# Kernel tuning notes

Hardware: AMD Instinct MI355X
Metric: run time of the kernel (lower is better)

The kernel has to match this reference:

```python
import jax, jax.numpy as jnp
import numpy as np

B, L, D = 4, 2048, 1024
NUM_HEADS = 1
HEAD_DIM = D // NUM_HEADS  # 1024


def setup_inputs() -> dict:
    key = jax.random.key(0)
    ks = jax.random.split(key, 12)
    s = 1.0 / np.sqrt(D)
    return {
        "query": jax.random.normal(ks[0], (B, L, D), jnp.float32),
        "key": jax.random.normal(ks[1], (B, L, D), jnp.float32),
        "value": jax.random.normal(ks[2], (B, L, D), jnp.float32),
        "mask": jax.random.randint(ks[3], (B, 1, L, L), 0, 2, jnp.int32),
        "Wq": jax.random.uniform(ks[4], (D, D * NUM_HEADS), jnp.float32, -s, s),
        "bq": jnp.zeros((D * NUM_HEADS,), jnp.float32),
        "Wk": jax.random.uniform(ks[5], (D, D * NUM_HEADS), jnp.float32, -s, s),
        "bk": jnp.zeros((D * NUM_HEADS,), jnp.float32),
        "Wv": jax.random.uniform(ks[6], (D, D * NUM_HEADS), jnp.float32, -s, s),
        "bv": jnp.zeros((D * NUM_HEADS,), jnp.float32),
        "Wo": jax.random.uniform(ks[7], (D * NUM_HEADS, D), jnp.float32, -s, s),
        "bo": jnp.zeros((D,), jnp.float32),
    }


def reference(query, key, value, mask, Wq, bq, Wk, bk, Wv, bv, Wo, bo):
    b, lq = query.shape[0], query.shape[1]
    lk = key.shape[1]
    # project and split heads: (B, L, H, Dh) -> (B, H, L, Dh)
    Q = (query @ Wq + bq).reshape(b, lq, NUM_HEADS, HEAD_DIM).transpose(0, 2, 1, 3)
    K = (key @ Wk + bk).reshape(b, lk, NUM_HEADS, HEAD_DIM).transpose(0, 2, 1, 3)
    V = (value @ Wv + bv).reshape(b, lk, NUM_HEADS, HEAD_DIM).transpose(0, 2, 1, 3)
    scale = 1.0 / jnp.sqrt(jnp.float32(HEAD_DIM))
    scores = jnp.einsum("bhqd,bhkd->bhqk", Q, K) * scale  # (B,H,Lq,Lk)
    scores = jnp.where(mask == 0, jnp.float32(-1e20), scores)
    attn = jax.nn.softmax(scores, axis=-1)
    out = jnp.einsum("bhqk,bhkd->bhqd", attn, V)  # (B,H,Lq,Dh)
    out = out.transpose(0, 2, 1, 3).reshape(b, lq, NUM_HEADS * HEAD_DIM)
    return out @ Wo + bo
```

## Files before the change

### kernel.cpp

```cpp
#include <hip/hip_runtime.h>

#define B_ 4
#define L_ 2048
#define D_ 1024
#define M_FLAT (B_*L_)
#define NE_ ((size_t)M_FLAT * D_)
#define WE_ ((size_t)D_ * D_)

typedef unsigned short bf16_t;
typedef __attribute__((ext_vector_type(8))) short bf16x8;
typedef __attribute__((ext_vector_type(4))) float f32x4;

__device__ __forceinline__ bf16_t f2bf(float f) {
  union { float f; unsigned int u; } c; c.f = f;
  unsigned int u = c.u;
  unsigned int r = (u + 0x7fffu + ((u >> 16) & 1u)) >> 16;
  return (bf16_t)r;
}
__device__ __forceinline__ float bf2f(bf16_t h) {
  union { unsigned int u; float f; } c; c.u = ((unsigned int)h) << 16;
  return c.f;
}

__device__ __forceinline__ void gload_lds16(const bf16_t* g, bf16_t* l) {
  __builtin_amdgcn_global_load_lds(
      (const __attribute__((address_space(1))) unsigned int*)g,
      (__attribute__((address_space(3))) unsigned int*)l, 16, 0, 0);
}

#define BARRIER() do { asm volatile("" ::: "memory"); \
                       __builtin_amdgcn_s_barrier();  \
                       asm volatile("" ::: "memory"); } while (0)

__global__ __launch_bounds__(256) void prep_cvt(const float* __restrict__ q,
                                                const float* __restrict__ k,
                                                const float* __restrict__ v,
                                                const float* __restrict__ wv,
                                                bf16_t* __restrict__ xq,
                                                bf16_t* __restrict__ wvb) {
  const float* in; bf16_t* out; size_t li;
  int b = blockIdx.x;
  if (b < 4096)       { in = q;  out = xq;            li = (size_t)b * 256 + threadIdx.x; }
  else if (b < 8192)  { in = k;  out = xq + NE_;      li = (size_t)(b - 4096) * 256 + threadIdx.x; }
  else if (b < 12288) { in = v;  out = xq + 2 * NE_;  li = (size_t)(b - 8192) * 256 + threadIdx.x; }
  else                { in = wv; out = wvb;           li = (size_t)(b - 12288) * 256 + threadIdx.x; }
  const float4* p = (const float4*)in + li * 2;
  float4 a = p[0], bb = p[1];
  union { bf16_t h[8]; uint4 u; } r;
  r.h[0] = f2bf(a.x); r.h[1] = f2bf(a.y); r.h[2] = f2bf(a.z); r.h[3] = f2bf(a.w);
  r.h[4] = f2bf(bb.x); r.h[5] = f2bf(bb.y); r.h[6] = f2bf(bb.z); r.h[7] = f2bf(bb.w);
  ((uint4*)out)[li] = r.u;
}

__global__ __launch_bounds__(256) void transpose_cvt3(const float* __restrict__ Wq,
                                                      const float* __restrict__ Wk,
                                                      const float* __restrict__ Wo,
                                                      bf16_t* __restrict__ outbase) {
  __shared__ float t[32][33];
  int zz = blockIdx.z;
  const float* Wsrc = (zz == 0) ? Wq : (zz == 1) ? Wk : Wo;
  bf16_t* Wt = outbase + (size_t)(zz == 2 ? 3 : zz) * WE_;
  int c0 = blockIdx.x * 32, r0 = blockIdx.y * 32;
  int tx = threadIdx.x, ty = threadIdx.y;
#pragma unroll
  for (int i = 0; i < 4; i++)
    t[ty + i * 8][tx] = Wsrc[(size_t)(r0 + ty + i * 8) * D_ + c0 + tx];
  __syncthreads();
#pragma unroll
  for (int i = 0; i < 4; i++)
    Wt[(size_t)(c0 + ty + i * 8) * D_ + r0 + tx] = f2bf(t[tx][ty + i * 8]);
}

__global__ __launch_bounds__(256) void c2_kernel(const float* __restrict__ bv,
                                                 const float* __restrict__ Wo,
                                                 float* __restrict__ c2) {
  int j = blockIdx.x * 256 + threadIdx.x;
  float s = 0.f;
  for (int k = 0; k < D_; k++) s += bv[k] * Wo[(size_t)k * D_ + j];
  c2[j] = s;
}

__global__ __launch_bounds__(256) void pack_mask(const int* __restrict__ mask,
                                                 unsigned long long* __restrict__ bm) {
  size_t gid = (size_t)blockIdx.x * 256 + threadIdx.x;
  int mi = mask[gid];
  unsigned long long b = __ballot(mi != 0);
  if ((threadIdx.x & 63) == 0) bm[gid >> 6] = b;
}

__global__ __launch_bounds__(256) void reduce_rsum(const float* __restrict__ rsp,
                                                   float* __restrict__ rs) {
  int r = blockIdx.x * 256 + threadIdx.x;
  float s = 0.f;
#pragma unroll
  for (int j = 0; j < 32; j++) s += rsp[(size_t)r * 32 + j];
  rs[r] = fmaxf(s, 1e-30f);
}

#define MODE_PROJ 0
#define MODE_S    1
#define MODE_FIN  2
#define MODE_TR   3

template <int BM, int MODE>
__global__ __launch_bounds__(512, 2)
void g8(const bf16_t* __restrict__ Abase, int lda, long strA,
        const bf16_t* __restrict__ Bbase, int ldb, long strB,
        void* __restrict__ outp, long strO, int ldo,
        const float* __restrict__ x0, const float* __restrict__ x1,
        const float* __restrict__ x2,
        const void* __restrict__ auxp, float* __restrict__ rsp,
        int K) {
  constexpr int WROWS = BM / 2;
  constexpr int QAF   = WROWS / 32;
  constexpr int MFR   = WROWS / 16;
  constexpr int AL    = BM / 128;
  constexpr int BL    = 2;
  constexpr int AHB   = WROWS * 128;
  constexpr int BUFB  = (BM + 256) * 128;
  extern __shared__ __align__(16) char smem[];

  const int tid = threadIdx.x, lane = tid & 63, w = tid >> 6;
  const int wm = w >> 2, wn = w & 3;
  const int fr = lane & 15, fs = lane >> 4;
  const int z = blockIdx.z;

  int gx = gridDim.x, nxy = gx * gridDim.y;
  int lin = blockIdx.y * gx + blockIdx.x;
  if ((nxy & 7) == 0) { int q = nxy >> 3; lin = (lin & 7) * q + (lin >> 3); }
  const int xb = lin % gx;
  const int mbase = (lin / gx) * BM, nbase = xb * 256;

  const bf16_t* A  = Abase + (size_t)z * strA;
  const bf16_t* Bt = Bbase + (size_t)z * strB;

  int offA[2][2], offB[2][2];
#pragma unroll
  for (int h = 0; h < 2; h++)
#pragma unroll
    for (int i = 0; i < 2; i++) {
      int c = i * 512 + tid, row = c >> 3;
      int sg = (c & 7) ^ (row & 7);
      if (i < AL) offA[h][i] = (mbase + h * WROWS + row) * lda + sg * 8;
      offB[h][i] = (nbase + h * 128 + row) * ldb + sg * 8;
    }

  const int swz0 = (fs ^ (fr & 7)) * 16;
  const int swz1 = ((4 + fs) ^ (fr & 7)) * 16;

  bf16x8 af[QAF][2], bfv[2][2][2];
  f32x4 acc[MFR][4] = {};

#define STAGE_A(h, kt, bsel) do {                                             \
    char* hb_ = smem + (bsel) * BUFB + (h) * AHB;                             \
    _Pragma("unroll")                                                         \
    for (int i_ = 0; i_ < AL; ++i_)                                           \
      gload_lds16(A + offA[h][i_] + (kt) * 64,                                \
                  (bf16_t*)(hb_ + (i_ * 512 + tid) * 16));                    \
  } while (0)
#define STAGE_B(h, kt, bsel) do {                                             \
    char* hb_ = smem + (bsel) * BUFB + BM * 128 + (h) * 16384;                \
    _Pragma("unroll")                                                         \
    for (int i_ = 0; i_ < BL; ++i_)                                           \
      gload_lds16(Bt + offB[h][i_] + (kt) * 64,                               \
                  (bf16_t*)(hb_ + (i_ * 512 + tid) * 16));                    \
  } while (0)
#define LOAD_A(bsel, mh) do {                                                 \
    const char* ab_ = smem + (bsel) * BUFB + (wm * WROWS) * 128;              \
    _Pragma("unroll")                                                         \
    for (int i_ = 0; i_ < QAF; ++i_) {                                        \
      int rb_ = ((mh) * (WROWS / 2) + i_ * 16 + fr) * 128;                    \
      af[i_][0] = *(const bf16x8*)(ab_ + rb_ + swz0);                         \
      af[i_][1] = *(const bf16x8*)(ab_ + rb_ + swz1);                         \
    }                                                                         \
  } while (0)
#define LOAD_B(bsel, nh) do {                                                 \
    const char* bb_ = smem + (bsel) * BUFB + BM * 128 + (wn * 64) * 128;      \
    _Pragma("unroll")                                                         \
    for (int j_ = 0; j_ < 2; ++j_) {                                          \
      int rb_ = ((nh) * 32 + j_ * 16 + fr) * 128;                             \
      bfv[nh][j_][0] = *(const bf16x8*)(bb_ + rb_ + swz0);                    \
      bfv[nh][j_][1] = *(const bf16x8*)(bb_ + rb_ + swz1);                    \
    }                                                                         \
  } while (0)
#define MFMA_Q(mh, nh) do {                                                   \
    __builtin_amdgcn_s_setprio(1);                                            \
    _Pragma("unroll")                                                         \
    for (int i_ = 0; i_ < QAF; ++i_)                                          \
    _Pragma("unroll")                                                         \
    for (int j_ = 0; j_ < 2; ++j_) {                                          \
      acc[(mh)*QAF + i_][(nh)*2 + j_] = __builtin_amdgcn_mfma_f32_16x16x32_bf16( \
          af[i_][0], bfv[nh][j_][0], acc[(mh)*QAF + i_][(nh)*2 + j_], 0, 0, 0);  \
      acc[(mh)*QAF + i_][(nh)*2 + j_] = __builtin_amdgcn_mfma_f32_16x16x32_bf16( \
          af[i_][1], bfv[nh][j_][1], acc[(mh)*QAF + i_][(nh)*2 + j_], 0, 0, 0);  \
    }                                                                         \
    __builtin_amdgcn_s_setprio(0);                                            \
  } while (0)
#define VMWN() do {                                                           \
    if constexpr (AL == 2) asm volatile("s_waitcnt vmcnt(8)" ::: "memory");   \
    else                   asm volatile("s_waitcnt vmcnt(6)" ::: "memory");   \
  } while (0)

  const int NK = K >> 6, NI = NK >> 1;

  STAGE_B(0, 0, 0); STAGE_B(1, 0, 0); STAGE_A(0, 0, 0); STAGE_A(1, 0, 0);
  STAGE_B(0, 1, 1); STAGE_B(1, 1, 1); STAGE_A(0, 1, 1); STAGE_A(1, 1, 1);
  VMWN(); BARRIER();

  for (int it = 0; it < NI; ++it) {
    const int ta = (2 * it + 2 < NK) ? 2 * it + 2 : NK - 1;
    const int tb = (2 * it + 3 < NK) ? 2 * it + 3 : NK - 1;
    LOAD_A(0, 0); LOAD_B(0, 0); MFMA_Q(0, 0);
    LOAD_B(0, 1);               MFMA_Q(0, 1);
    LOAD_A(0, 1);               MFMA_Q(1, 1);
                                MFMA_Q(1, 0);
    BARRIER();
    STAGE_B(0, ta, 0); STAGE_B(1, ta, 0); STAGE_A(0, ta, 0); STAGE_A(1, ta, 0);
    VMWN();
    BARRIER();
    LOAD_A(1, 0); LOAD_B(1, 0); MFMA_Q(0, 0);
    LOAD_B(1, 1);               MFMA_Q(0, 1);
    LOAD_A(1, 1);               MFMA_Q(1, 1);
                                MFMA_Q(1, 0);
    BARRIER();
    STAGE_B(0, tb, 1); STAGE_B(1, tb, 1); STAGE_A(0, tb, 1); STAGE_A(1, tb, 1);
    VMWN();
    BARRIER();
  }
  asm volatile("s_waitcnt vmcnt(0)" ::: "memory");

  const int r0 = mbase + wm * WROWS;
  const int c0 = nbase + wn * 64;

  if constexpr (MODE == MODE_PROJ) {
    BARRIER();
    char* ep = smem + w * AHB;
    if (z < 2) {
      bf16_t* o = (bf16_t*)outp + (size_t)z * strO;
      const float* bias = (z == 0) ? x0 : x1;
      const float scale = (z == 0) ? 0.03125f : 1.0f;
#pragma unroll
      for (int nf = 0; nf < 4; ++nf) {
        float bv = bias[c0 + nf * 16 + fr];
#pragma unroll
        for (int mf = 0; mf < MFR; ++mf)
#pragma unroll
          for (int jj = 0; jj < 4; ++jj) {
            int row = mf * 16 + fs * 4 + jj;
            int slot = (nf * 2 + (fr >> 3)) ^ ((row >> 1) & 7);
            *(bf16_t*)(ep + row * 128 + slot * 16 + (fr & 7) * 2) =
                f2bf((acc[mf][nf][jj] + bv) * scale);
          }
      }
      asm volatile("s_waitcnt lgkmcnt(0)" ::: "memory");
      const int rl = lane >> 3, sl = lane & 7;
#pragma unroll
      for (int i = 0; i < WROWS / 8; ++i) {
        int row = i * 8 + rl;
        int slot = sl ^ ((row >> 1) & 7);
        uint4 vv = *(const uint4*)(ep + row * 128 + slot * 16);
        *(uint4*)&o[(size_t)(r0 + row) * ldo + c0 + sl * 8] = vv;
      }
    } else {
      bf16_t* ob = (bf16_t*)auxp;
      const int bidx = r0 >> 11, rb = r0 & (L_ - 1);
      ob += (size_t)bidx * D_ * L_;
#pragma unroll
      for (int nf = 0; nf < 4; ++nf) {
        int coll = nf * 16 + fr;
        float bv = x2[c0 + coll];
        int xm = (coll & (WROWS / 8 - 1)) << 3;
#pragma unroll
        for (int mf = 0; mf < MFR; ++mf) {
          int rbase = mf * 16 + fs * 4;
          union { bf16_t h[4]; uint2 u; } pk;
#pragma unroll
          for (int jj = 0; jj < 4; ++jj) pk.h[jj] = f2bf(acc[mf][nf][jj] + bv);
          *(uint2*)(ep + coll * (WROWS * 2) + 2 * (rbase ^ xm)) = pk.u;
        }
      }
      asm volatile("s_waitcnt lgkmcnt(0)" ::: "memory");
      constexpr int LPC = WROWS / 8;
      constexpr int CPI = 64 / LPC;
      const int colr = lane / LPC;
      const int rc = (lane % LPC) * 8;
#pragma unroll
      for (int i2 = 0; i2 < LPC; ++i2) {
        int coll = i2 * CPI + colr;
        int xm = (coll & (WROWS / 8 - 1)) << 3;
        uint4 vv = *(const uint4*)(ep + coll * (WROWS * 2) + 2 * (rc ^ xm));
        *(uint4*)&ob[(size_t)(c0 + coll) * L_ + rb + rc] = vv;
      }
    }
  } else if constexpr (MODE == MODE_TR) {
    BARRIER();
    char* ep = smem + w * AHB;
    bf16_t* ob = (bf16_t*)outp;
#pragma unroll
    for (int nf = 0; nf < 4; ++nf) {
      int coll = nf * 16 + fr;
      int xm = (coll & (WROWS / 8 - 1)) << 3;
#pragma unroll
      for (int mf = 0; mf < MFR; ++mf) {
        int rbase = mf * 16 + fs * 4;
        union { bf16_t h[4]; uint2 u; } pk;
#pragma unroll
        for (int jj = 0; jj < 4; ++jj) pk.h[jj] = f2bf(acc[mf][nf][jj]);
        *(uint2*)(ep + coll * (WROWS * 2) + 2 * (rbase ^ xm)) = pk.u;
      }
    }
    asm volatile("s_waitcnt lgkmcnt(0)" ::: "memory");
    constexpr int LPC = WROWS / 8;
    constexpr int CPI = 64 / LPC;
    const int colr = lane / LPC;
    const int rc = (lane % LPC) * 8;
#pragma unroll
    for (int i2 = 0; i2 < LPC; ++i2) {
      int coll = i2 * CPI + colr;
      int xm = (coll & (WROWS / 8 - 1)) << 3;
      uint4 vv = *(const uint4*)(ep + coll * (WROWS * 2) + 2 * (rc ^ xm));
      *(uint4*)&ob[(size_t)(c0 + coll) * ldo + r0 + rc] = vv;
    }
  } else if constexpr (MODE == MODE_S) {
    BARRIER();
    char* ep = smem + w * AHB;
    bf16_t* o = (bf16_t*)outp + (size_t)z * strO;
    const unsigned long long* bw =
        (const unsigned long long*)auxp +
        ((size_t)z * L_ + r0) * 32 + (c0 >> 6);
#pragma unroll
    for (int mf = 0; mf < MFR; ++mf) {
#pragma unroll
      for (int jj = 0; jj < 4; ++jj) {
        int row = mf * 16 + fs * 4 + jj;
        unsigned long long wd = bw[(size_t)row * 32];
        float psum = 0.f;
#pragma unroll
        for (int nf = 0; nf < 4; ++nf) {
          int cbit = nf * 16 + fr;
          float e = ((wd >> cbit) & 1ull) ? __expf(acc[mf][nf][jj]) : 0.0f;
          bf16_t eb = f2bf(e);
          psum += bf2f(eb);
          int slot = (nf * 2 + (fr >> 3)) ^ ((row >> 1) & 7);
          *(bf16_t*)(ep + row * 128 + slot * 16 + (fr & 7) * 2) = eb;
        }
#pragma unroll
        for (int off = 8; off; off >>= 1) psum += __shfl_xor(psum, off, 16);
        if (fr == 0)
          rsp[((size_t)z * L_ + r0 + row) * 32 + xb * 4 + wn] = psum;
      }
    }
    asm volatile("s_waitcnt lgkmcnt(0)" ::: "memory");
    const int rl = lane >> 3, sl = lane & 7;
#pragma unroll
    for (int i = 0; i < WROWS / 8; ++i) {
      int row = i * 8 + rl;
      int slot = sl ^ ((row >> 1) & 7);
      uint4 vv = *(const uint4*)(ep + row * 128 + slot * 16);
      *(uint4*)&o[(size_t)(r0 + row) * ldo + c0 + sl * 8] = vv;
    }
  } else {
    float* o = (float*)outp + (size_t)z * strO;
    const float* rs = x0 + (size_t)z * L_;
#pragma unroll
    for (int mf = 0; mf < MFR; ++mf) {
#pragma unroll
      for (int jj = 0; jj < 4; ++jj) {
        int r = r0 + mf * 16 + fs * 4 + jj;
        float inv = 1.0f / rs[r];
#pragma unroll
        for (int nf = 0; nf < 4; ++nf) {
          int c = c0 + nf * 16 + fr;
          o[(size_t)r * ldo + c] = acc[mf][nf][jj] * inv + x1[c];
        }
      }
    }
  }
#undef STAGE_A
#undef STAGE_B
#undef LOAD_A
#undef LOAD_B
#undef MFMA_Q
#undef VMWN
}

extern "C" void kernel_launch(void* const* d_in, const int* in_sizes, int n_in,
                              void* d_out, int out_size, void* d_ws, size_t ws_size,
                              hipStream_t stream) {
  const float* query = (const float*)d_in[0];
  const float* keyi  = (const float*)d_in[1];
  const float* value = (const float*)d_in[2];
  const int*   mask  = (const int*)d_in[3];
  const float* Wq = (const float*)d_in[4];
  const float* bq = (const float*)d_in[5];
  const float* Wk = (const float*)d_in[6];
  const float* bk = (const float*)d_in[7];
  const float* Wv = (const float*)d_in[8];
  const float* bv = (const float*)d_in[9];
  const float* Wo = (const float*)d_in[10];
  const float* bo = (const float*)d_in[11];

  bf16_t* ws = (bf16_t*)d_ws;
  bf16_t* XQ   = ws;
  bf16_t* XK   = ws + NE_;
  bf16_t* XV   = ws + 2 * NE_;
  bf16_t* WQT  = ws + 3 * NE_;
  bf16_t* WKT  = WQT + WE_;
  bf16_t* W2T  = WKT + WE_;
  bf16_t* WOT  = W2T + WE_;
  bf16_t* WVb  = WOT + WE_;
  bf16_t* Qb   = WVb + WE_;
  bf16_t* Kb   = Qb + NE_;
  bf16_t* VWt  = Kb + NE_;
  float*  rsump= (float*)(VWt + NE_);
  float*  c2p  = rsump + (size_t)B_ * L_;
  float*  rspart = c2p + D_;
  unsigned long long* bmask =
      (unsigned long long*)(rspart + (size_t)B_ * L_ * 32);
  bf16_t* Sb   = ws;

  hipFuncSetAttribute((const void*)g8<128, MODE_PROJ>,
                      hipFuncAttributeMaxDynamicSharedMemorySize, 98304);
  hipFuncSetAttribute((const void*)g8<256, MODE_S>,
                      hipFuncAttributeMaxDynamicSharedMemorySize, 131072);
  hipFuncSetAttribute((const void*)g8<128, MODE_TR>,
                      hipFuncAttributeMaxDynamicSharedMemorySize, 98304);
  hipFuncSetAttribute((const void*)g8<128, MODE_FIN>,
                      hipFuncAttributeMaxDynamicSharedMemorySize, 98304);

  prep_cvt<<<dim3(12800), dim3(256), 0, stream>>>(query, keyi, value, Wv, XQ, WVb);
  pack_mask<<<dim3(65536), dim3(256), 0, stream>>>(mask, bmask);
  transpose_cvt3<<<dim3(32, 32, 3), dim3(32, 8), 0, stream>>>(Wq, Wk, Wo, WQT);
  c2_kernel<<<dim3(4), dim3(256), 0, stream>>>(bv, Wo, c2p);
  g8<128, MODE_TR><<<dim3(4, 8, 1), 512, 98304, stream>>>(
      WVb, D_, 0, WOT, D_, 0, W2T, 0, D_,
      nullptr, nullptr, nullptr, nullptr, nullptr, D_);
  g8<128, MODE_PROJ><<<dim3(4, 64, 3), 512, 98304, stream>>>(
      XQ, D_, (long)NE_, WQT, D_, (long)WE_, Qb, (long)NE_, D_,
      bq, bk, c2p, VWt, nullptr, D_);
  g8<256, MODE_S><<<dim3(8, 8, 4), 512, 131072, stream>>>(
      Qb, D_, (long)L_ * D_, Kb, D_, (long)L_ * D_, Sb, (long)L_ * L_, L_,
      nullptr, nullptr, nullptr, bmask, rspart, D_);
  reduce_rsum<<<dim3(32), dim3(256), 0, stream>>>(rspart, rsump);
  g8<128, MODE_FIN><<<dim3(4, 16, 4), 512, 98304, stream>>>(
      Sb, L_, (long)L_ * L_, VWt, L_, (long)D_ * L_, d_out, (long)L_ * D_, D_,
      rsump, bo, nullptr, nullptr, nullptr, L_);
}
```

Measured before the change: 264.2 us.

## Fuse fp32-to-bf16 input conversion into projection GEMM and split-K the Wv·Wo product

Removes the separate prep_cvt pass. The projection GEMM now loads the fp32 query/key/value tiles directly into registers, converts them to bf16 and writes them to LDS, so the extra read-write of bf16 copies of the inputs is gone. The small Wv·Wo weight-product GEMM, which previously ran on only 32 blocks, becomes an 8-way split-K into fp32 partials followed by a reduce-and-transpose kernel. Wv conversion moves into the weight transpose kernel. The trade-off is that A-tile staging now goes through registers and costs more VGPRs, with a heavier global-read path inside the main GEMM loop.

```diff
diff --git a/kernel.cpp b/kernel.cpp
--- a/kernel.cpp
+++ b/kernel.cpp
@@ -32,36 +32,26 @@
                        __builtin_amdgcn_s_barrier();  \
                        asm volatile("" ::: "memory"); } while (0)
 
-__global__ __launch_bounds__(256) void prep_cvt(const float* __restrict__ q,
-                                                const float* __restrict__ k,
-                                                const float* __restrict__ v,
-                                                const float* __restrict__ wv,
-                                                bf16_t* __restrict__ xq,
-                                                bf16_t* __restrict__ wvb) {
-  const float* in; bf16_t* out; size_t li;
-  int b = blockIdx.x;
-  if (b < 4096)       { in = q;  out = xq;            li = (size_t)b * 256 + threadIdx.x; }
-  else if (b < 8192)  { in = k;  out = xq + NE_;      li = (size_t)(b - 4096) * 256 + threadIdx.x; }
-  else if (b < 12288) { in = v;  out = xq + 2 * NE_;  li = (size_t)(b - 8192) * 256 + threadIdx.x; }
-  else                { in = wv; out = wvb;           li = (size_t)(b - 12288) * 256 + threadIdx.x; }
-  const float4* p = (const float4*)in + li * 2;
-  float4 a = p[0], bb = p[1];
-  union { bf16_t h[8]; uint4 u; } r;
-  r.h[0] = f2bf(a.x); r.h[1] = f2bf(a.y); r.h[2] = f2bf(a.z); r.h[3] = f2bf(a.w);
-  r.h[4] = f2bf(bb.x); r.h[5] = f2bf(bb.y); r.h[6] = f2bf(bb.z); r.h[7] = f2bf(bb.w);
-  ((uint4*)out)[li] = r.u;
-}
-
-__global__ __launch_bounds__(256) void transpose_cvt3(const float* __restrict__ Wq,
+__global__ __launch_bounds__(256) void transpose_cvt4(const float* __restrict__ Wq,
                                                       const float* __restrict__ Wk,
                                                       const float* __restrict__ Wo,
+                                                      const float* __restrict__ Wv,
                                                       bf16_t* __restrict__ outbase) {
   __shared__ float t[32][33];
   int zz = blockIdx.z;
+  int c0 = blockIdx.x * 32, r0 = blockIdx.y * 32;
+  int tx = threadIdx.x, ty = threadIdx.y;
+  if (zz == 3) {
+    bf16_t* o = outbase + 4 * WE_;
+#pragma unroll
+    for (int i = 0; i < 4; i++) {
+      size_t idx = (size_t)(r0 + ty + i * 8) * D_ + c0 + tx;
+      o[idx] = f2bf(Wv[idx]);
+    }
+    return;
+  }
   const float* Wsrc = (zz == 0) ? Wq : (zz == 1) ? Wk : Wo;
   bf16_t* Wt = outbase + (size_t)(zz == 2 ? 3 : zz) * WE_;
-  int c0 = blockIdx.x * 32, r0 = blockIdx.y * 32;
-  int tx = threadIdx.x, ty = threadIdx.y;
 #pragma unroll
   for (int i = 0; i < 4; i++)
     t[ty + i * 8][tx] = Wsrc[(size_t)(r0 + ty + i * 8) * D_ + c0 + tx];
@@ -97,10 +87,29 @@
   rs[r] = fmaxf(s, 1e-30f);
 }
 
+__global__ __launch_bounds__(256) void w2_reduce(const float* __restrict__ pw,
+                                                 bf16_t* __restrict__ w2t) {
+  __shared__ float t[32][33];
+  int c0 = blockIdx.x * 32, r0 = blockIdx.y * 32;
+  int tx = threadIdx.x, ty = threadIdx.y;
+#pragma unroll
+  for (int i = 0; i < 4; i++) {
+    size_t idx = (size_t)(r0 + ty + i * 8) * D_ + c0 + tx;
+    float s = 0.f;
+#pragma unroll
+    for (int zz = 0; zz < 8; zz++) s += pw[(size_t)zz * WE_ + idx];
+    t[ty + i * 8][tx] = s;
+  }
+  __syncthreads();
+#pragma unroll
+  for (int i = 0; i < 4; i++)
+    w2t[(size_t)(c0 + ty + i * 8) * D_ + r0 + tx] = f2bf(t[tx][ty + i * 8]);
+}
+
 #define MODE_PROJ 0
 #define MODE_S    1
 #define MODE_FIN  2
-#define MODE_TR   3
+#define MODE_TRK  3
 
 template <int BM, int MODE>
 __global__ __launch_bounds__(512, 2)
@@ -110,6 +119,8 @@
         const float* __restrict__ x0, const float* __restrict__ x1,
         const float* __restrict__ x2,
         const void* __restrict__ auxp, float* __restrict__ rsp,
+        const float* __restrict__ fq, const float* __restrict__ fk,
+        const float* __restrict__ fv,
         int K) {
   constexpr int WROWS = BM / 2;
   constexpr int QAF   = WROWS / 32;
@@ -133,6 +144,8 @@
 
   const bf16_t* A  = Abase + (size_t)z * strA;
   const bf16_t* Bt = Bbase + (size_t)z * strB;
+  const float* FA = (MODE == MODE_PROJ)
+                        ? ((z == 0) ? fq : (z == 1) ? fk : fv) : nullptr;
 
   int offA[2][2], offB[2][2];
 #pragma unroll
@@ -150,6 +163,7 @@
 
   bf16x8 af[QAF][2], bfv[2][2][2];
   f32x4 acc[MFR][4] = {};
+  float4 apl[2][2];
 
 #define STAGE_A(h, kt, bsel) do {                                             \
     char* hb_ = smem + (bsel) * BUFB + (h) * AHB;                             \
@@ -164,6 +178,19 @@
     for (int i_ = 0; i_ < BL; ++i_)                                           \
       gload_lds16(Bt + offB[h][i_] + (kt) * 64,                               \
                   (bf16_t*)(hb_ + (i_ * 512 + tid) * 16));                    \
+  } while (0)
+#define AFP_LOAD(h, kt) do {                                                  \
+    const float* s_ = FA + offA[h][0] + (kt) * 64;                            \
+    apl[h][0] = *(const float4*)s_;                                           \
+    apl[h][1] = *(const float4*)(s_ + 4);                                     \
+  } while (0)
+#define AFP_WRITE(h, bsel) do {                                               \
+    union { bf16_t hh[8]; uint4 q; } ub_;                                     \
+    ub_.hh[0] = f2bf(apl[h][0].x); ub_.hh[1] = f2bf(apl[h][0].y);             \
+    ub_.hh[2] = f2bf(apl[h][0].z); ub_.hh[3] = f2bf(apl[h][0].w);             \
+    ub_.hh[4] = f2bf(apl[h][1].x); ub_.hh[5] = f2bf(apl[h][1].y);             \
+    ub_.hh[6] = f2bf(apl[h][1].z); ub_.hh[7] = f2bf(apl[h][1].w);             \
+    *(uint4*)(smem + (bsel) * BUFB + (h) * AHB + tid * 16) = ub_.q;           \
   } while (0)
 #define LOAD_A(bsel, mh) do {                                                 \
     const char* ab_ = smem + (bsel) * BUFB + (wm * WROWS) * 128;              \
@@ -200,31 +227,60 @@
     if constexpr (AL == 2) asm volatile("s_waitcnt vmcnt(8)" ::: "memory");   \
     else                   asm volatile("s_waitcnt vmcnt(6)" ::: "memory");   \
   } while (0)
+#define LGKM0() asm volatile("s_waitcnt lgkmcnt(0)" ::: "memory")
 
   const int NK = K >> 6, NI = NK >> 1;
 
-  STAGE_B(0, 0, 0); STAGE_B(1, 0, 0); STAGE_A(0, 0, 0); STAGE_A(1, 0, 0);
-  STAGE_B(0, 1, 1); STAGE_B(1, 1, 1); STAGE_A(0, 1, 1); STAGE_A(1, 1, 1);
-  VMWN(); BARRIER();
+  if constexpr (MODE == MODE_PROJ) {
+    AFP_LOAD(0, 0); AFP_LOAD(1, 0);
+    STAGE_B(0, 0, 0); STAGE_B(1, 0, 0);
+    AFP_WRITE(0, 0); AFP_WRITE(1, 0);
+    AFP_LOAD(0, 1); AFP_LOAD(1, 1);
+    STAGE_B(0, 1, 1); STAGE_B(1, 1, 1);
+    AFP_WRITE(0, 1); AFP_WRITE(1, 1);
+    LGKM0();
+    asm volatile("s_waitcnt vmcnt(4)" ::: "memory");
+    BARRIER();
+  } else {
+    STAGE_B(0, 0, 0); STAGE_B(1, 0, 0); STAGE_A(0, 0, 0); STAGE_A(1, 0, 0);
+    STAGE_B(0, 1, 1); STAGE_B(1, 1, 1); STAGE_A(0, 1, 1); STAGE_A(1, 1, 1);
+    VMWN(); BARRIER();
+  }
 
   for (int it = 0; it < NI; ++it) {
     const int ta = (2 * it + 2 < NK) ? 2 * it + 2 : NK - 1;
     const int tb = (2 * it + 3 < NK) ? 2 * it + 3 : NK - 1;
+    if constexpr (MODE == MODE_PROJ) { AFP_LOAD(0, ta); AFP_LOAD(1, ta); }
     LOAD_A(0, 0); LOAD_B(0, 0); MFMA_Q(0, 0);
     LOAD_B(0, 1);               MFMA_Q(0, 1);
     LOAD_A(0, 1);               MFMA_Q(1, 1);
                                 MFMA_Q(1, 0);
     BARRIER();
-    STAGE_B(0, ta, 0); STAGE_B(1, ta, 0); STAGE_A(0, ta, 0); STAGE_A(1, ta, 0);
-    VMWN();
-    BARRIER();
+    STAGE_B(0, ta, 0); STAGE_B(1, ta, 0);
+    if constexpr (MODE == MODE_PROJ) {
+      AFP_WRITE(0, 0); AFP_WRITE(1, 0);
+      LGKM0();
+      asm volatile("s_waitcnt vmcnt(4)" ::: "memory");
+    } else {
+      STAGE_A(0, ta, 0); STAGE_A(1, ta, 0);
+      VMWN();
+    }
+    BARRIER();
+    if constexpr (MODE == MODE_PROJ) { AFP_LOAD(0, tb); AFP_LOAD(1, tb); }
     LOAD_A(1, 0); LOAD_B(1, 0); MFMA_Q(0, 0);
     LOAD_B(1, 1);               MFMA_Q(0, 1);
     LOAD_A(1, 1);               MFMA_Q(1, 1);
                                 MFMA_Q(1, 0);
     BARRIER();
-    STAGE_B(0, tb, 1); STAGE_B(1, tb, 1); STAGE_A(0, tb, 1); STAGE_A(1, tb, 1);
-    VMWN();
+    STAGE_B(0, tb, 1); STAGE_B(1, tb, 1);
+    if constexpr (MODE == MODE_PROJ) {
+      AFP_WRITE(0, 1); AFP_WRITE(1, 1);
+      LGKM0();
+      asm volatile("s_waitcnt vmcnt(4)" ::: "memory");
+    } else {
+      STAGE_A(0, tb, 1); STAGE_A(1, tb, 1);
+      VMWN();
+    }
     BARRIER();
   }
   asm volatile("s_waitcnt vmcnt(0)" ::: "memory");
@@ -252,7 +308,7 @@
                 f2bf((acc[mf][nf][jj] + bv) * scale);
           }
       }
-      asm volatile("s_waitcnt lgkmcnt(0)" ::: "memory");
+      LGKM0();
       const int rl = lane >> 3, sl = lane & 7;
 #pragma unroll
       for (int i = 0; i < WROWS / 8; ++i) {
@@ -279,7 +335,7 @@
           *(uint2*)(ep + coll * (WROWS * 2) + 2 * (rbase ^ xm)) = pk.u;
         }
       }
-      asm volatile("s_waitcnt lgkmcnt(0)" ::: "memory");
+      LGKM0();
       constexpr int LPC = WROWS / 8;
       constexpr int CPI = 64 / LPC;
       const int colr = lane / LPC;
@@ -292,34 +348,17 @@
         *(uint4*)&ob[(size_t)(c0 + coll) * L_ + rb + rc] = vv;
       }
     }
-  } else if constexpr (MODE == MODE_TR) {
-    BARRIER();
-    char* ep = smem + w * AHB;
-    bf16_t* ob = (bf16_t*)outp;
-#pragma unroll
-    for (int nf = 0; nf < 4; ++nf) {
-      int coll = nf * 16 + fr;
-      int xm = (coll & (WROWS / 8 - 1)) << 3;
-#pragma unroll
-      for (int mf = 0; mf < MFR; ++mf) {
-        int rbase = mf * 16 + fs * 4;
-        union { bf16_t h[4]; uint2 u; } pk;
-#pragma unroll
-        for (int jj = 0; jj < 4; ++jj) pk.h[jj] = f2bf(acc[mf][nf][jj]);
-        *(uint2*)(ep + coll * (WROWS * 2) + 2 * (rbase ^ xm)) = pk.u;
-      }
-    }
-    asm volatile("s_waitcnt lgkmcnt(0)" ::: "memory");
-    constexpr int LPC = WROWS / 8;
-    constexpr int CPI = 64 / LPC;
-    const int colr = lane / LPC;
-    const int rc = (lane % LPC) * 8;
-#pragma unroll
-    for (int i2 = 0; i2 < LPC; ++i2) {
-      int coll = i2 * CPI + colr;
-      int xm = (coll & (WROWS / 8 - 1)) << 3;
-      uint4 vv = *(const uint4*)(ep + coll * (WROWS * 2) + 2 * (rc ^ xm));
-      *(uint4*)&ob[(size_t)(c0 + coll) * ldo + r0 + rc] = vv;
+  } else if constexpr (MODE == MODE_TRK) {
+    float* o = (float*)outp + (size_t)z * strO;
+#pragma unroll
+    for (int mf = 0; mf < MFR; ++mf) {
+#pragma unroll
+      for (int jj = 0; jj < 4; ++jj) {
+        int r = r0 + mf * 16 + fs * 4 + jj;
+#pragma unroll
+        for (int nf = 0; nf < 4; ++nf)
+          o[(size_t)r * ldo + c0 + nf * 16 + fr] = acc[mf][nf][jj];
+      }
     }
   } else if constexpr (MODE == MODE_S) {
     BARRIER();
@@ -350,7 +389,7 @@
           rsp[((size_t)z * L_ + r0 + row) * 32 + xb * 4 + wn] = psum;
       }
     }
-    asm volatile("s_waitcnt lgkmcnt(0)" ::: "memory");
+    LGKM0();
     const int rl = lane >> 3, sl = lane & 7;
 #pragma unroll
     for (int i = 0; i < WROWS / 8; ++i) {
@@ -378,10 +417,13 @@
   }
 #undef STAGE_A
 #undef STAGE_B
+#undef AFP_LOAD
+#undef AFP_WRITE
 #undef LOAD_A
 #undef LOAD_B
 #undef MFMA_Q
 #undef VMWN
+#undef LGKM0
 }
 
 extern "C" void kernel_launch(void* const* d_in, const int* in_sizes, int n_in,
@@ -401,10 +443,10 @@
   const float* bo = (const float*)d_in[11];
 
   bf16_t* ws = (bf16_t*)d_ws;
-  bf16_t* XQ   = ws;
-  bf16_t* XK   = ws + NE_;
-  bf16_t* XV   = ws + 2 * NE_;
-  bf16_t* WQT  = ws + 3 * NE_;
+  const size_t SBE = (size_t)B_ * L_ * L_;
+  bf16_t* Sb   = ws;
+  float*  pW2  = (float*)ws;
+  bf16_t* WQT  = ws + SBE;
   bf16_t* WKT  = WQT + WE_;
   bf16_t* W2T  = WKT + WE_;
   bf16_t* WOT  = W2T + WE_;
@@ -417,32 +459,35 @@
   float*  rspart = c2p + D_;
   unsigned long long* bmask =
       (unsigned long long*)(rspart + (size_t)B_ * L_ * 32);
-  bf16_t* Sb   = ws;
 
   hipFuncSetAttribute((const void*)g8<128, MODE_PROJ>,
                       hipFuncAttributeMaxDynamicSharedMemorySize, 98304);
   hipFuncSetAttribute((const void*)g8<256, MODE_S>,
                       hipFuncAttributeMaxDynamicSharedMemorySize, 131072);
-  hipFuncSetAttribute((const void*)g8<128, MODE_TR>,
+  hipFuncSetAttribute((const void*)g8<128, MODE_TRK>,
                       hipFuncAttributeMaxDynamicSharedMemorySize, 98304);
   hipFuncSetAttribute((const void*)g8<128, MODE_FIN>,
                       hipFuncAttributeMaxDynamicSharedMemorySize, 98304);
 
-  prep_cvt<<<dim3(12800), dim3(256), 0, stream>>>(query, keyi, value, Wv, XQ, WVb);
   pack_mask<<<dim3(65536), dim3(256), 0, stream>>>(mask, bmask);
-  transpose_cvt3<<<dim3(32, 32, 3), dim3(32, 8), 0, stream>>>(Wq, Wk, Wo, WQT);
+  transpose_cvt4<<<dim3(32, 32, 4), dim3(32, 8), 0, stream>>>(Wq, Wk, Wo, Wv, WQT);
   c2_kernel<<<dim3(4), dim3(256), 0, stream>>>(bv, Wo, c2p);
-  g8<128, MODE_TR><<<dim3(4, 8, 1), 512, 98304, stream>>>(
-      WVb, D_, 0, WOT, D_, 0, W2T, 0, D_,
-      nullptr, nullptr, nullptr, nullptr, nullptr, D_);
+  g8<128, MODE_TRK><<<dim3(4, 8, 8), 512, 98304, stream>>>(
+      WVb, D_, 128, WOT, D_, 128, pW2, (long)WE_, D_,
+      nullptr, nullptr, nullptr, nullptr, nullptr,
+      nullptr, nullptr, nullptr, 128);
+  w2_reduce<<<dim3(32, 32), dim3(32, 8), 0, stream>>>(pW2, W2T);
   g8<128, MODE_PROJ><<<dim3(4, 64, 3), 512, 98304, stream>>>(
-      XQ, D_, (long)NE_, WQT, D_, (long)WE_, Qb, (long)NE_, D_,
-      bq, bk, c2p, VWt, nullptr, D_);
+      nullptr, D_, 0, WQT, D_, (long)WE_, Qb, (long)NE_, D_,
+      bq, bk, c2p, VWt, nullptr,
+      query, keyi, value, D_);
   g8<256, MODE_S><<<dim3(8, 8, 4), 512, 131072, stream>>>(
       Qb, D_, (long)L_ * D_, Kb, D_, (long)L_ * D_, Sb, (long)L_ * L_, L_,
-      nullptr, nullptr, nullptr, bmask, rspart, D_);
+      nullptr, nullptr, nullptr, bmask, rspart,
+      nullptr, nullptr, nullptr, D_);
   reduce_rsum<<<dim3(32), dim3(256), 0, stream>>>(rspart, rsump);
   g8<128, MODE_FIN><<<dim3(4, 16, 4), 512, 98304, stream>>>(
       Sb, L_, (long)L_ * L_, VWt, L_, (long)D_ * L_, d_out, (long)L_ * D_, D_,
-      rsump, bo, nullptr, nullptr, nullptr, L_);
-}
+      rsump, bo, nullptr, nullptr, nullptr,
+      nullptr, nullptr, nullptr, L_);
+}
```

Result: slower. 296.7 us (+12.3%).

## Split Wv·Wo weight product over K and reduce partials in separate kernel

Applied to the files above, without the earlier changes.

The small 1024x1024x1024 weight-product GEMM, which previously ran as only 32 workgroups, is now split along K into 8 slices of 128. This gives 256 workgroups that write fp32 partials into scratch, and a new kernel sums, transposes and converts them to bf16. The Wv bf16 conversion moves from prep_cvt into the weight-transpose kernel as a fourth z-slice. The aim is to fill the GPU during this serial-latency stage, at the cost of extra fp32 partial traffic and one more launch.

```diff
diff --git a/kernel.cpp b/kernel.cpp
--- a/kernel.cpp
+++ b/kernel.cpp
@@ -35,15 +35,12 @@
 __global__ __launch_bounds__(256) void prep_cvt(const float* __restrict__ q,
                                                 const float* __restrict__ k,
                                                 const float* __restrict__ v,
-                                                const float* __restrict__ wv,
-                                                bf16_t* __restrict__ xq,
-                                                bf16_t* __restrict__ wvb) {
+                                                bf16_t* __restrict__ xq) {
   const float* in; bf16_t* out; size_t li;
   int b = blockIdx.x;
   if (b < 4096)       { in = q;  out = xq;            li = (size_t)b * 256 + threadIdx.x; }
   else if (b < 8192)  { in = k;  out = xq + NE_;      li = (size_t)(b - 4096) * 256 + threadIdx.x; }
-  else if (b < 12288) { in = v;  out = xq + 2 * NE_;  li = (size_t)(b - 8192) * 256 + threadIdx.x; }
-  else                { in = wv; out = wvb;           li = (size_t)(b - 12288) * 256 + threadIdx.x; }
+  else                { in = v;  out = xq + 2 * NE_;  li = (size_t)(b - 8192) * 256 + threadIdx.x; }
   const float4* p = (const float4*)in + li * 2;
   float4 a = p[0], bb = p[1];
   union { bf16_t h[8]; uint4 u; } r;
@@ -52,16 +49,26 @@
   ((uint4*)out)[li] = r.u;
 }
 
-__global__ __launch_bounds__(256) void transpose_cvt3(const float* __restrict__ Wq,
+__global__ __launch_bounds__(256) void transpose_cvt4(const float* __restrict__ Wq,
                                                       const float* __restrict__ Wk,
                                                       const float* __restrict__ Wo,
+                                                      const float* __restrict__ Wv,
                                                       bf16_t* __restrict__ outbase) {
   __shared__ float t[32][33];
   int zz = blockIdx.z;
+  int c0 = blockIdx.x * 32, r0 = blockIdx.y * 32;
+  int tx = threadIdx.x, ty = threadIdx.y;
+  if (zz == 3) {
+    bf16_t* o = outbase + 4 * WE_;
+#pragma unroll
+    for (int i = 0; i < 4; i++) {
+      size_t idx = (size_t)(r0 + ty + i * 8) * D_ + c0 + tx;
+      o[idx] = f2bf(Wv[idx]);
+    }
+    return;
+  }
   const float* Wsrc = (zz == 0) ? Wq : (zz == 1) ? Wk : Wo;
   bf16_t* Wt = outbase + (size_t)(zz == 2 ? 3 : zz) * WE_;
-  int c0 = blockIdx.x * 32, r0 = blockIdx.y * 32;
-  int tx = threadIdx.x, ty = threadIdx.y;
 #pragma unroll
   for (int i = 0; i < 4; i++)
     t[ty + i * 8][tx] = Wsrc[(size_t)(r0 + ty + i * 8) * D_ + c0 + tx];
@@ -97,10 +104,29 @@
   rs[r] = fmaxf(s, 1e-30f);
 }
 
+__global__ __launch_bounds__(256) void w2_reduce(const float* __restrict__ pw,
+                                                 bf16_t* __restrict__ w2t) {
+  __shared__ float t[32][33];
+  int c0 = blockIdx.x * 32, r0 = blockIdx.y * 32;
+  int tx = threadIdx.x, ty = threadIdx.y;
+#pragma unroll
+  for (int i = 0; i < 4; i++) {
+    size_t idx = (size_t)(r0 + ty + i * 8) * D_ + c0 + tx;
+    float s = 0.f;
+#pragma unroll
+    for (int zz = 0; zz < 8; zz++) s += pw[(size_t)zz * WE_ + idx];
+    t[ty + i * 8][tx] = s;
+  }
+  __syncthreads();
+#pragma unroll
+  for (int i = 0; i < 4; i++)
+    w2t[(size_t)(c0 + ty + i * 8) * D_ + r0 + tx] = f2bf(t[tx][ty + i * 8]);
+}
+
 #define MODE_PROJ 0
 #define MODE_S    1
 #define MODE_FIN  2
-#define MODE_TR   3
+#define MODE_TRK  3
 
 template <int BM, int MODE>
 __global__ __launch_bounds__(512, 2)
@@ -200,6 +226,7 @@
     if constexpr (AL == 2) asm volatile("s_waitcnt vmcnt(8)" ::: "memory");   \
     else                   asm volatile("s_waitcnt vmcnt(6)" ::: "memory");   \
   } while (0)
+#define LGKM0() asm volatile("s_waitcnt lgkmcnt(0)" ::: "memory")
 
   const int NK = K >> 6, NI = NK >> 1;
 
@@ -252,7 +279,7 @@
                 f2bf((acc[mf][nf][jj] + bv) * scale);
           }
       }
-      asm volatile("s_waitcnt lgkmcnt(0)" ::: "memory");
+      LGKM0();
       const int rl = lane >> 3, sl = lane & 7;
 #pragma unroll
       for (int i = 0; i < WROWS / 8; ++i) {
@@ -279,7 +306,7 @@
           *(uint2*)(ep + coll * (WROWS * 2) + 2 * (rbase ^ xm)) = pk.u;
         }
       }
-      asm volatile("s_waitcnt lgkmcnt(0)" ::: "memory");
+      LGKM0();
       constexpr int LPC = WROWS / 8;
       constexpr int CPI = 64 / LPC;
       const int colr = lane / LPC;
@@ -292,34 +319,17 @@
         *(uint4*)&ob[(size_t)(c0 + coll) * L_ + rb + rc] = vv;
       }
     }
-  } else if constexpr (MODE == MODE_TR) {
-    BARRIER();
-    char* ep = smem + w * AHB;
-    bf16_t* ob = (bf16_t*)outp;
-#pragma unroll
-    for (int nf = 0; nf < 4; ++nf) {
-      int coll = nf * 16 + fr;
-      int xm = (coll & (WROWS / 8 - 1)) << 3;
-#pragma unroll
-      for (int mf = 0; mf < MFR; ++mf) {
-        int rbase = mf * 16 + fs * 4;
-        union { bf16_t h[4]; uint2 u; } pk;
-#pragma unroll
-        for (int jj = 0; jj < 4; ++jj) pk.h[jj] = f2bf(acc[mf][nf][jj]);
-        *(uint2*)(ep + coll * (WROWS * 2) + 2 * (rbase ^ xm)) = pk.u;
-      }
-    }
-    asm volatile("s_waitcnt lgkmcnt(0)" ::: "memory");
-    constexpr int LPC = WROWS / 8;
-    constexpr int CPI = 64 / LPC;
-    const int colr = lane / LPC;
-    const int rc = (lane % LPC) * 8;
-#pragma unroll
-    for (int i2 = 0; i2 < LPC; ++i2) {
-      int coll = i2 * CPI + colr;
-      int xm = (coll & (WROWS / 8 - 1)) << 3;
-      uint4 vv = *(const uint4*)(ep + coll * (WROWS * 2) + 2 * (rc ^ xm));
-      *(uint4*)&ob[(size_t)(c0 + coll) * ldo + r0 + rc] = vv;
+  } else if constexpr (MODE == MODE_TRK) {
+    float* o = (float*)outp + (size_t)z * strO;
+#pragma unroll
+    for (int mf = 0; mf < MFR; ++mf) {
+#pragma unroll
+      for (int jj = 0; jj < 4; ++jj) {
+        int r = r0 + mf * 16 + fs * 4 + jj;
+#pragma unroll
+        for (int nf = 0; nf < 4; ++nf)
+          o[(size_t)r * ldo + c0 + nf * 16 + fr] = acc[mf][nf][jj];
+      }
     }
   } else if constexpr (MODE == MODE_S) {
     BARRIER();
@@ -350,7 +360,7 @@
           rsp[((size_t)z * L_ + r0 + row) * 32 + xb * 4 + wn] = psum;
       }
     }
-    asm volatile("s_waitcnt lgkmcnt(0)" ::: "memory");
+    LGKM0();
     const int rl = lane >> 3, sl = lane & 7;
 #pragma unroll
     for (int i = 0; i < WROWS / 8; ++i) {
@@ -382,6 +392,7 @@
 #undef LOAD_B
 #undef MFMA_Q
 #undef VMWN
+#undef LGKM0
 }
 
 extern "C" void kernel_launch(void* const* d_in, const int* in_sizes, int n_in,
@@ -418,23 +429,25 @@
   unsigned long long* bmask =
       (unsigned long long*)(rspart + (size_t)B_ * L_ * 32);
   bf16_t* Sb   = ws;
+  float*  pW2  = (float*)Qb;
 
   hipFuncSetAttribute((const void*)g8<128, MODE_PROJ>,
                       hipFuncAttributeMaxDynamicSharedMemorySize, 98304);
   hipFuncSetAttribute((const void*)g8<256, MODE_S>,
                       hipFuncAttributeMaxDynamicSharedMemorySize, 131072);
-  hipFuncSetAttribute((const void*)g8<128, MODE_TR>,
+  hipFuncSetAttribute((const void*)g8<128, MODE_TRK>,
                       hipFuncAttributeMaxDynamicSharedMemorySize, 98304);
   hipFuncSetAttribute((const void*)g8<128, MODE_FIN>,
                       hipFuncAttributeMaxDynamicSharedMemorySize, 98304);
 
-  prep_cvt<<<dim3(12800), dim3(256), 0, stream>>>(query, keyi, value, Wv, XQ, WVb);
+  prep_cvt<<<dim3(12288), dim3(256), 0, stream>>>(query, keyi, value, XQ);
   pack_mask<<<dim3(65536), dim3(256), 0, stream>>>(mask, bmask);
-  transpose_cvt3<<<dim3(32, 32, 3), dim3(32, 8), 0, stream>>>(Wq, Wk, Wo, WQT);
+  transpose_cvt4<<<dim3(32, 32, 4), dim3(32, 8), 0, stream>>>(Wq, Wk, Wo, Wv, WQT);
   c2_kernel<<<dim3(4), dim3(256), 0, stream>>>(bv, Wo, c2p);
-  g8<128, MODE_TR><<<dim3(4, 8, 1), 512, 98304, stream>>>(
-      WVb, D_, 0, WOT, D_, 0, W2T, 0, D_,
-      nullptr, nullptr, nullptr, nullptr, nullptr, D_);
+  g8<128, MODE_TRK><<<dim3(4, 8, 8), 512, 98304, stream>>>(
+      WVb, D_, 128, WOT, D_, 128, pW2, (long)WE_, D_,
+      nullptr, nullptr, nullptr, nullptr, nullptr, 128);
+  w2_reduce<<<dim3(32, 32), dim3(32, 8), 0, stream>>>(pW2, W2T);
   g8<128, MODE_PROJ><<<dim3(4, 64, 3), 512, 98304, stream>>>(
       XQ, D_, (long)NE_, WQT, D_, (long)WE_, Qb, (long)NE_, D_,
       bq, bk, c2p, VWt, nullptr, D_);
```

Measured after the change: 267.2 us. No clear change (+1.1%).
